# Performance work log

Measured on AMD Instinct MI355X. Metric: run time of the kernel, lower is better.

## Reference

```python
import jax, jax.numpy as jnp
import numpy as np

N_NODES = 20000
N_EDGES = 640000
IN_DIM, HIDDEN, OUT_DIM = 128, 256, 64
EPS = 1e-12


def setup_inputs() -> dict:
    key = jax.random.key(0)
    ks = jax.random.split(key, 8)
    x = jax.random.normal(ks[0], (N_NODES, IN_DIM), dtype=jnp.float32)
    edge_src = jax.random.randint(ks[1], (N_EDGES,), 0, N_NODES, dtype=jnp.int32)
    edge_dst = jax.random.randint(ks[2], (N_EDGES,), 0, N_NODES, dtype=jnp.int32)
    s1 = 1.0 / np.sqrt(IN_DIM)
    s2 = 1.0 / np.sqrt(HIDDEN)
    W1 = jax.random.uniform(ks[3], (IN_DIM, HIDDEN), jnp.float32, -s1, s1)
    b1 = jax.random.uniform(ks[4], (HIDDEN,), jnp.float32, -s1, s1)
    W2 = jax.random.uniform(ks[5], (HIDDEN, OUT_DIM), jnp.float32, -s2, s2)
    b2 = jax.random.uniform(ks[6], (OUT_DIM,), jnp.float32, -s2, s2)
    return {"x": x, "edge_src": edge_src, "edge_dst": edge_dst,
            "W1": W1, "b1": b1, "W2": W2, "b2": b2}


def _agnn_layer(h, src, dst, n_nodes):
    # AGNN propagation with beta = 1 (non-trainable buffer in source module):
    # out_i = sum_j softmax_j(cos(h_i, h_j)) * h_j over neighbors j (incl. self-loop)
    hn = h * jax.lax.rsqrt(jnp.sum(h * h, axis=-1, keepdims=True) + EPS)
    logits = jnp.sum(hn[src] * hn[dst], axis=-1)            # [E] cosine similarity
    m = jax.ops.segment_max(logits, dst, num_segments=n_nodes)
    e = jnp.exp(logits - m[dst])
    z = jax.ops.segment_sum(e, dst, num_segments=n_nodes)
    alpha = e / z[dst]                                       # per-dst softmax
    return jax.ops.segment_sum(alpha[:, None] * h[src], dst, num_segments=n_nodes)


def reference(x, edge_src, edge_dst, W1, b1, W2, b2):
    n = x.shape[0]
    loop = jnp.arange(n, dtype=edge_src.dtype)
    src = jnp.concatenate([edge_src, loop])
    dst = jnp.concatenate([edge_dst, loop])
    h = jax.nn.relu(x @ W1 + b1)
    for _ in range(4):
        h = jax.nn.relu(_agnn_layer(h, src, dst, n))
    return h @ W2 + b2
```

## Files before the change

### kernel.cpp

```cpp
#include <hip/hip_runtime.h>

#define N_NODES 20000
#define N_EDGES 640000
#define E_TOT   (N_EDGES + N_NODES)
#define IN_DIM  128
#define HIDDEN  256
#define OUT_DIM 64
#define LOG2E 1.4426950408889634f
#define NBIN 1024

typedef __attribute__((ext_vector_type(2))) float f32x2;

__device__ __forceinline__ unsigned short f2bf(float f) {
    union { float f; unsigned int i; } x; x.f = f;
    unsigned int u = x.i;
    return (unsigned short)((u + 0x7fffu + ((u >> 16) & 1u)) >> 16);
}
__device__ __forceinline__ f32x2 up2(unsigned int p) {
    f32x2 r;
    r.x = __uint_as_float(p << 16);
    r.y = __uint_as_float(p & 0xffff0000u);
    return r;
}
__device__ __forceinline__ unsigned int pk2(float a, float b) {
    return (unsigned int)f2bf(a) | ((unsigned int)f2bf(b) << 16);
}


__global__ void zero_all_kernel(int* __restrict__ cnt, int* __restrict__ hcur) {
    int i = blockIdx.x * blockDim.x + threadIdx.x;
    if (i < N_NODES) cnt[i] = 0;
    if (i < NBIN) hcur[i] = 0;
}

__global__ void count_kernel(const int* __restrict__ edge_dst, int* __restrict__ cnt) {
    int i = blockIdx.x * blockDim.x + threadIdx.x;
    if (i >= E_TOT) return;
    int d = (i < N_EDGES) ? edge_dst[i] : (i - N_EDGES);
    atomicAdd(&cnt[d], 1);
}

__global__ __launch_bounds__(1024) void scan_fused_kernel(int* __restrict__ cnt,
                                                          int* __restrict__ indptr,
                                                          int* __restrict__ hbase) {
    const int T = 1024;
    const int C = (N_NODES + T - 1) / T;
    __shared__ int sums[T];
    __shared__ int hist[T];
    int t = threadIdx.x;
    hist[t] = 0;
    __syncthreads();
    int base = t * C;
    int local[C];
    int s = 0;
#pragma unroll
    for (int i = 0; i < C; i++) {
        int idx = base + i;
        int v = 0;
        if (idx < N_NODES) {
            v = cnt[idx];
            int k = (v > NBIN - 1) ? (NBIN - 1) : v;
            atomicAdd(&hist[NBIN - 1 - k], 1);
        }
        local[i] = s;
        s += v;
    }
    sums[t] = s;
    __syncthreads();
    for (int off = 1; off < T; off <<= 1) {
        int v = (t >= off) ? sums[t - off] : 0;
        __syncthreads();
        sums[t] += v;
        __syncthreads();
    }
    int prefix = (t == 0) ? 0 : sums[t - 1];
#pragma unroll
    for (int i = 0; i < C; i++) {
        int idx = base + i;
        if (idx < N_NODES) {
            indptr[idx] = prefix + local[i];
            cnt[idx] = 0;
        }
    }
    if (t == T - 1) indptr[N_NODES] = prefix + s;
    __syncthreads();
    int hv = hist[t];
    sums[t] = hv;
    __syncthreads();
    for (int off = 1; off < T; off <<= 1) {
        int v = (t >= off) ? sums[t - off] : 0;
        __syncthreads();
        sums[t] += v;
        __syncthreads();
    }
    hbase[t] = sums[t] - hv;
}

__global__ void scatter_both_kernel(const int* __restrict__ edge_src,
                                    const int* __restrict__ edge_dst,
                                    const int* __restrict__ indptr,
                                    int* __restrict__ cnt,
                                    int* __restrict__ ssrc,
                                    const int* __restrict__ hbase,
                                    int* __restrict__ hcur,
                                    int* __restrict__ perm) {
    int i = blockIdx.x * blockDim.x + threadIdx.x;
    if (i < E_TOT) {
        int d, s;
        if (i < N_EDGES) { d = edge_dst[i]; s = edge_src[i]; }
        else             { d = i - N_EDGES; s = d; }
        int pos = indptr[d] + atomicAdd(&cnt[d], 1);
        ssrc[pos] = s;
    } else if (i < E_TOT + N_NODES) {
        int nidx = i - E_TOT;
        int d = indptr[nidx + 1] - indptr[nidx];
        int k = (d > NBIN - 1) ? (NBIN - 1) : d;
        int key = NBIN - 1 - k;
        int pos = hbase[key] + atomicAdd(&hcur[key], 1);
        perm[pos] = nidx;
    }
}


__global__ __launch_bounds__(256) void gemm_bias_act(const float* __restrict__ A,
                                                     const float* __restrict__ B,
                                                     const float* __restrict__ bias,
                                                     float* __restrict__ C,
                                                     int M, int Nn, int K, int relu) {
    __shared__ float As[16][65];
    __shared__ float Bs[16][65];
    int tid = threadIdx.x;
    int tx = tid & 15, ty = tid >> 4;
    int row0 = blockIdx.x * 64, col0 = blockIdx.y * 64;
    float acc[4][4] = {};
    for (int k0 = 0; k0 < K; k0 += 16) {
        {
            int r_ = tid >> 2;
            int kq = (tid & 3) * 4;
            int gr = row0 + r_;
            float4 a4 = make_float4(0.f, 0.f, 0.f, 0.f);
            if (gr < M) a4 = *(const float4*)&A[(long)gr * K + k0 + kq];
            As[kq + 0][r_] = a4.x; As[kq + 1][r_] = a4.y;
            As[kq + 2][r_] = a4.z; As[kq + 3][r_] = a4.w;
        }
        {
            int kr = tid >> 4;
            int cq = (tid & 15) * 4;
            float4 b4 = *(const float4*)&B[(long)(k0 + kr) * Nn + col0 + cq];
            Bs[kr][cq + 0] = b4.x; Bs[kr][cq + 1] = b4.y;
            Bs[kr][cq + 2] = b4.z; Bs[kr][cq + 3] = b4.w;
        }
        __syncthreads();
#pragma unroll
        for (int kk = 0; kk < 16; kk++) {
            float a[4], b[4];
#pragma unroll
            for (int i = 0; i < 4; i++) a[i] = As[kk][ty * 4 + i];
#pragma unroll
            for (int j = 0; j < 4; j++) b[j] = Bs[kk][tx * 4 + j];
#pragma unroll
            for (int i = 0; i < 4; i++)
#pragma unroll
                for (int j = 0; j < 4; j++) acc[i][j] += a[i] * b[j];
        }
        __syncthreads();
    }
#pragma unroll
    for (int i = 0; i < 4; i++) {
        int gr = row0 + ty * 4 + i;
        if (gr >= M) continue;
#pragma unroll
        for (int j = 0; j < 4; j++) {
            int gc = col0 + tx * 4 + j;
            float v = acc[i][j] + bias[gc];
            if (relu) v = fmaxf(v, 0.f);
            C[(long)gr * Nn + gc] = v;
        }
    }
}


__global__ __launch_bounds__(256) void normalize0_kernel(const float* __restrict__ h,
                                                         unsigned short* __restrict__ hnb,
                                                         float* __restrict__ r) {
    int wid = threadIdx.x >> 6, lane = threadIdx.x & 63;
    int i = blockIdx.x * 4 + wid;
    const float4* h4 = (const float4*)(h + (long)i * HIDDEN);
    float4 v = h4[lane];
    float ss = v.x * v.x + v.y * v.y + v.z * v.z + v.w * v.w;
#pragma unroll
    for (int off = 32; off; off >>= 1) ss += __shfl_xor(ss, off);
    float rr = sqrtf(ss + 1e-12f);
    float ir = 1.f / rr;
    uint2 o;
    o.x = pk2(v.x * ir, v.y * ir);
    o.y = pk2(v.z * ir, v.w * ir);
    ((uint2*)(hnb + (long)i * HIDDEN))[lane] = o;
    if (lane == 0) r[i] = rr;
}


__global__ __launch_bounds__(256) void agnn_kernel(const unsigned short* __restrict__ hnb,
                                                   const float* __restrict__ rin,
                                                   const int* __restrict__ indptr,
                                                   const int* __restrict__ ssrc,
                                                   const int* __restrict__ perm,
                                                   unsigned short* __restrict__ hnout,
                                                   float* __restrict__ rout,
                                                   float* __restrict__ hout,
                                                   int write_hn) {
    int lane = threadIdx.x & 63;
    int wid  = threadIdx.x >> 6;
    int half = lane >> 5;
    int sub  = (lane >> 4) & 1;
    int gl   = lane & 15;
    int node = perm[blockIdx.x * 8 + wid * 2 + half];

    const uint4* tab4 = (const uint4*)hnb;
    long nb = (long)node * 32 + gl * 2;
    uint4 ha = tab4[nb], hb = tab4[nb + 1];
    f32x2 hd2[8];
    hd2[0] = up2(ha.x) * LOG2E; hd2[1] = up2(ha.y) * LOG2E;
    hd2[2] = up2(ha.z) * LOG2E; hd2[3] = up2(ha.w) * LOG2E;
    hd2[4] = up2(hb.x) * LOG2E; hd2[5] = up2(hb.y) * LOG2E;
    hd2[6] = up2(hb.z) * LOG2E; hd2[7] = up2(hb.w) * LOG2E;

    int beg = indptr[node], end = indptr[node + 1];
    int deg = end - beg;
    int c0  = (deg + 1) >> 1;
    int cnt = sub ? (deg - c0) : c0;
    int eb  = beg + (sub ? c0 : 0);
    int lim = (cnt > 0) ? (eb + cnt - 1) : beg;
    int nmax = max(cnt, __shfl_xor(cnt, 16));
    nmax = max(nmax, __shfl_xor(nmax, 32));

    f32x2 acc[8];
#pragma unroll
    for (int p = 0; p < 8; p++) acc[p] = (f32x2)0.f;
    float z = 0.f;

    int s0 = ssrc[(0 < cnt) ? eb : lim];
    int s1 = ssrc[min(eb + 1, lim)];
    long b0 = (long)s0 * 32 + gl * 2;
    uint4 v0a = tab4[b0], v0b = tab4[b0 + 1];
    float r0 = rin[s0];
    long b1 = (long)s1 * 32 + gl * 2;
    uint4 v1a = tab4[b1], v1b = tab4[b1 + 1];
    float r1 = rin[s1];
    int s2 = ssrc[min(eb + 2, lim)];

    for (int i = 0; i < nmax; i++) {
        uint4 ca = v0a, cb = v0b;
        float cr = r0;
        v0a = v1a; v0b = v1b; r0 = r1;
        long b2 = (long)s2 * 32 + gl * 2;
        v1a = tab4[b2]; v1b = tab4[b2 + 1];
        r1 = rin[s2];
        s2 = ssrc[min(eb + i + 3, lim)];

        f32x2 cf[8];
        cf[0] = up2(ca.x); cf[1] = up2(ca.y); cf[2] = up2(ca.z); cf[3] = up2(ca.w);
        cf[4] = up2(cb.x); cf[5] = up2(cb.y); cf[6] = up2(cb.z); cf[7] = up2(cb.w);
        f32x2 da = cf[0] * hd2[0];
        f32x2 db = cf[1] * hd2[1];
        da += cf[2] * hd2[2];  db += cf[3] * hd2[3];
        da += cf[4] * hd2[4];  db += cf[5] * hd2[5];
        da += cf[6] * hd2[6];  db += cf[7] * hd2[7];
        f32x2 d2 = da + db;
        float d = d2.x + d2.y;
        d += __shfl_xor(d, 1);
        d += __shfl_xor(d, 2);
        d += __shfl_xor(d, 4);
        d += __shfl_xor(d, 8);
        float w = (i < cnt) ? exp2f(d) : 0.f;
        z += w;
        float wr = w * cr;
#pragma unroll
        for (int p = 0; p < 8; p++) acc[p] += cf[p] * wr;
    }

    z += __shfl_xor(z, 16);
#pragma unroll
    for (int p = 0; p < 8; p++) {
        acc[p].x += __shfl_xor(acc[p].x, 16);
        acc[p].y += __shfl_xor(acc[p].y, 16);
    }

    float inv = 1.f / z;
    f32x2 o[8];
#pragma unroll
    for (int p = 0; p < 8; p++) {
        f32x2 t = acc[p] * inv;
        t.x = fmaxf(t.x, 0.f);
        t.y = fmaxf(t.y, 0.f);
        o[p] = t;
    }

    if (write_hn) {
        float ss = 0.f;
#pragma unroll
        for (int p = 0; p < 8; p++) ss += o[p].x * o[p].x + o[p].y * o[p].y;
        ss += __shfl_xor(ss, 1);
        ss += __shfl_xor(ss, 2);
        ss += __shfl_xor(ss, 4);
        ss += __shfl_xor(ss, 8);
        float rr = sqrtf(ss + 1e-12f);
        float ir = 1.f / rr;
        if (sub == 0) {
            uint4 oa, ob;
            oa.x = pk2(o[0].x * ir, o[0].y * ir);
            oa.y = pk2(o[1].x * ir, o[1].y * ir);
            oa.z = pk2(o[2].x * ir, o[2].y * ir);
            oa.w = pk2(o[3].x * ir, o[3].y * ir);
            ob.x = pk2(o[4].x * ir, o[4].y * ir);
            ob.y = pk2(o[5].x * ir, o[5].y * ir);
            ob.z = pk2(o[6].x * ir, o[6].y * ir);
            ob.w = pk2(o[7].x * ir, o[7].y * ir);
            uint4* outt = (uint4*)hnout;
            outt[nb] = oa;
            outt[nb + 1] = ob;
            if (gl == 0) rout[node] = rr;
        }
    } else {
        if (sub == 0) {
            float4* ho = (float4*)(hout + (long)node * HIDDEN + gl * 16);
            ho[0] = make_float4(o[0].x, o[0].y, o[1].x, o[1].y);
            ho[1] = make_float4(o[2].x, o[2].y, o[3].x, o[3].y);
            ho[2] = make_float4(o[4].x, o[4].y, o[5].x, o[5].y);
            ho[3] = make_float4(o[6].x, o[6].y, o[7].x, o[7].y);
        }
    }
}


extern "C" void kernel_launch(void* const* d_in, const int* in_sizes, int n_in,
                              void* d_out, int out_size, void* d_ws, size_t ws_size,
                              hipStream_t stream) {
    const float* x  = (const float*)d_in[0];
    const int* esrc = (const int*)d_in[1];
    const int* edst = (const int*)d_in[2];
    const float* W1 = (const float*)d_in[3];
    const float* b1 = (const float*)d_in[4];
    const float* W2 = (const float*)d_in[5];
    const float* b2 = (const float*)d_in[6];
    float* out = (float*)d_out;

    char* ws = (char*)d_ws;
    float*          h0     = (float*)(ws);
    unsigned short* hnA    = (unsigned short*)(ws + 20480000);
    unsigned short* hnB    = (unsigned short*)(ws + 30720000);
    float*          rA     = (float*)(ws + 40960000);
    float*          rB     = (float*)(ws + 41040000);
    int*            indptr = (int*)  (ws + 41120000);
    int*            cnt    = (int*)  (ws + 41200256);
    int*            ssrc   = (int*)  (ws + 41280256);
    int*            perm   = (int*)  (ws + 43920256);
    int*            hbase  = (int*)  (ws + 44000256);
    int*            hcur   = (int*)  (ws + 44004352);

    zero_all_kernel<<<(N_NODES + 255) / 256, 256, 0, stream>>>(cnt, hcur);
    count_kernel<<<(E_TOT + 255) / 256, 256, 0, stream>>>(edst, cnt);
    scan_fused_kernel<<<1, 1024, 0, stream>>>(cnt, indptr, hbase);
    scatter_both_kernel<<<(E_TOT + N_NODES + 255) / 256, 256, 0, stream>>>(
        esrc, edst, indptr, cnt, ssrc, hbase, hcur, perm);

    dim3 g1((N_NODES + 63) / 64, HIDDEN / 64);
    gemm_bias_act<<<g1, 256, 0, stream>>>(x, W1, b1, h0, N_NODES, HIDDEN, IN_DIM, 1);

    normalize0_kernel<<<N_NODES / 4, 256, 0, stream>>>(h0, hnA, rA);

    int nblk = N_NODES / 8;
    agnn_kernel<<<nblk, 256, 0, stream>>>(hnA, rA, indptr, ssrc, perm, hnB, rB, h0, 1);
    agnn_kernel<<<nblk, 256, 0, stream>>>(hnB, rB, indptr, ssrc, perm, hnA, rA, h0, 1);
    agnn_kernel<<<nblk, 256, 0, stream>>>(hnA, rA, indptr, ssrc, perm, hnB, rB, h0, 1);
    agnn_kernel<<<nblk, 256, 0, stream>>>(hnB, rB, indptr, ssrc, perm, hnA, rA, h0, 0);

    dim3 g2((N_NODES + 63) / 64, OUT_DIM / 64);
    gemm_bias_act<<<g2, 256, 0, stream>>>(h0, W2, b2, out, N_NODES, OUT_DIM, HIDDEN, 0);
}
```

Baseline: 358.4 us.

## Shard CSR-build counters and assign one wave per node in AGNN

```diff
diff --git a/kernel.cpp b/kernel.cpp
--- a/kernel.cpp
+++ b/kernel.cpp
@@ -8,6 +8,7 @@
 #define OUT_DIM 64
 #define LOG2E 1.4426950408889634f
 #define NBIN 1024
+#define NSHARD 8
 
 typedef __attribute__((ext_vector_type(2))) float f32x2;
 
@@ -27,26 +28,27 @@
 }
 
 
-__global__ void zero_all_kernel(int* __restrict__ cnt, int* __restrict__ hcur) {
+__global__ void zero_all_kernel(int* __restrict__ cnt8, int* __restrict__ hcur) {
     int i = blockIdx.x * blockDim.x + threadIdx.x;
-    if (i < N_NODES) cnt[i] = 0;
+    if (i < NSHARD * N_NODES) cnt8[i] = 0;
     if (i < NBIN) hcur[i] = 0;
 }
 
-__global__ void count_kernel(const int* __restrict__ edge_dst, int* __restrict__ cnt) {
+__global__ void count_kernel(const int* __restrict__ edge_dst, int* __restrict__ cnt8) {
     int i = blockIdx.x * blockDim.x + threadIdx.x;
     if (i >= E_TOT) return;
+    int shard = blockIdx.x & (NSHARD - 1);
     int d = (i < N_EDGES) ? edge_dst[i] : (i - N_EDGES);
-    atomicAdd(&cnt[d], 1);
-}
-
-__global__ __launch_bounds__(1024) void scan_fused_kernel(int* __restrict__ cnt,
+    atomicAdd(&cnt8[shard * N_NODES + d], 1);
+}
+
+__global__ __launch_bounds__(1024) void scan_fused_kernel(int* __restrict__ cnt8,
                                                           int* __restrict__ indptr,
                                                           int* __restrict__ hbase) {
     const int T = 1024;
     const int C = (N_NODES + T - 1) / T;
     __shared__ int sums[T];
-    __shared__ int hist[T];
+    __shared__ int hist[NBIN];
     int t = threadIdx.x;
     hist[t] = 0;
     __syncthreads();
@@ -56,14 +58,15 @@
 #pragma unroll
     for (int i = 0; i < C; i++) {
         int idx = base + i;
-        int v = 0;
+        int deg = 0;
         if (idx < N_NODES) {
-            v = cnt[idx];
-            int k = (v > NBIN - 1) ? (NBIN - 1) : v;
+#pragma unroll
+            for (int s8 = 0; s8 < NSHARD; s8++) deg += cnt8[s8 * N_NODES + idx];
+            int k = (deg > NBIN - 1) ? (NBIN - 1) : deg;
             atomicAdd(&hist[NBIN - 1 - k], 1);
         }
         local[i] = s;
-        s += v;
+        s += deg;
     }
     sums[t] = s;
     __syncthreads();
@@ -78,8 +81,15 @@
     for (int i = 0; i < C; i++) {
         int idx = base + i;
         if (idx < N_NODES) {
-            indptr[idx] = prefix + local[i];
-            cnt[idx] = 0;
+            int ip = prefix + local[i];
+            indptr[idx] = ip;
+            int running = ip;
+#pragma unroll
+            for (int s8 = 0; s8 < NSHARD; s8++) {
+                int c = cnt8[s8 * N_NODES + idx];
+                cnt8[s8 * N_NODES + idx] = running;
+                running += c;
+            }
         }
     }
     if (t == T - 1) indptr[N_NODES] = prefix + s;
@@ -99,17 +109,18 @@
 __global__ void scatter_both_kernel(const int* __restrict__ edge_src,
                                     const int* __restrict__ edge_dst,
                                     const int* __restrict__ indptr,
-                                    int* __restrict__ cnt,
+                                    int* __restrict__ cnt8,
                                     int* __restrict__ ssrc,
                                     const int* __restrict__ hbase,
                                     int* __restrict__ hcur,
                                     int* __restrict__ perm) {
     int i = blockIdx.x * blockDim.x + threadIdx.x;
     if (i < E_TOT) {
+        int shard = blockIdx.x & (NSHARD - 1);
         int d, s;
         if (i < N_EDGES) { d = edge_dst[i]; s = edge_src[i]; }
         else             { d = i - N_EDGES; s = d; }
-        int pos = indptr[d] + atomicAdd(&cnt[d], 1);
+        int pos = atomicAdd(&cnt8[shard * N_NODES + d], 1);
         ssrc[pos] = s;
     } else if (i < E_TOT + N_NODES) {
         int nidx = i - E_TOT;
@@ -211,10 +222,9 @@
                                                    int write_hn) {
     int lane = threadIdx.x & 63;
     int wid  = threadIdx.x >> 6;
-    int half = lane >> 5;
-    int sub  = (lane >> 4) & 1;
+    int sub  = lane >> 4;
     int gl   = lane & 15;
-    int node = perm[blockIdx.x * 8 + wid * 2 + half];
+    int node = perm[blockIdx.x * 4 + wid];
 
     const uint4* tab4 = (const uint4*)hnb;
     long nb = (long)node * 32 + gl * 2;
@@ -227,9 +237,9 @@
 
     int beg = indptr[node], end = indptr[node + 1];
     int deg = end - beg;
-    int c0  = (deg + 1) >> 1;
-    int cnt = sub ? (deg - c0) : c0;
-    int eb  = beg + (sub ? c0 : 0);
+    int qb  = deg >> 2, rem = deg & 3;
+    int cnt = qb + (sub < rem ? 1 : 0);
+    int eb  = beg + sub * qb + min(sub, rem);
     int lim = (cnt > 0) ? (eb + cnt - 1) : beg;
     int nmax = max(cnt, __shfl_xor(cnt, 16));
     nmax = max(nmax, __shfl_xor(nmax, 32));
@@ -280,10 +290,13 @@
     }
 
     z += __shfl_xor(z, 16);
+    z += __shfl_xor(z, 32);
 #pragma unroll
     for (int p = 0; p < 8; p++) {
         acc[p].x += __shfl_xor(acc[p].x, 16);
         acc[p].y += __shfl_xor(acc[p].y, 16);
+        acc[p].x += __shfl_xor(acc[p].x, 32);
+        acc[p].y += __shfl_xor(acc[p].y, 32);
     }
 
     float inv = 1.f / z;
@@ -352,24 +365,24 @@
     float*          rA     = (float*)(ws + 40960000);
     float*          rB     = (float*)(ws + 41040000);
     int*            indptr = (int*)  (ws + 41120000);
-    int*            cnt    = (int*)  (ws + 41200256);
-    int*            ssrc   = (int*)  (ws + 41280256);
-    int*            perm   = (int*)  (ws + 43920256);
-    int*            hbase  = (int*)  (ws + 44000256);
-    int*            hcur   = (int*)  (ws + 44004352);
-
-    zero_all_kernel<<<(N_NODES + 255) / 256, 256, 0, stream>>>(cnt, hcur);
-    count_kernel<<<(E_TOT + 255) / 256, 256, 0, stream>>>(edst, cnt);
-    scan_fused_kernel<<<1, 1024, 0, stream>>>(cnt, indptr, hbase);
+    int*            cnt8   = (int*)  (ws + 41200256);
+    int*            ssrc   = (int*)  (ws + 41840256);
+    int*            perm   = (int*)  (ws + 44480256);
+    int*            hbase  = (int*)  (ws + 44560256);
+    int*            hcur   = (int*)  (ws + 44564352);
+
+    zero_all_kernel<<<(NSHARD * N_NODES + 255) / 256, 256, 0, stream>>>(cnt8, hcur);
+    count_kernel<<<(E_TOT + 255) / 256, 256, 0, stream>>>(edst, cnt8);
+    scan_fused_kernel<<<1, 1024, 0, stream>>>(cnt8, indptr, hbase);
     scatter_both_kernel<<<(E_TOT + N_NODES + 255) / 256, 256, 0, stream>>>(
-        esrc, edst, indptr, cnt, ssrc, hbase, hcur, perm);
+        esrc, edst, indptr, cnt8, ssrc, hbase, hcur, perm);
 
     dim3 g1((N_NODES + 63) / 64, HIDDEN / 64);
     gemm_bias_act<<<g1, 256, 0, stream>>>(x, W1, b1, h0, N_NODES, HIDDEN, IN_DIM, 1);
 
     normalize0_kernel<<<N_NODES / 4, 256, 0, stream>>>(h0, hnA, rA);
 
-    int nblk = N_NODES / 8;
+    int nblk = N_NODES / 4;
     agnn_kernel<<<nblk, 256, 0, stream>>>(hnA, rA, indptr, ssrc, perm, hnB, rB, h0, 1);
     agnn_kernel<<<nblk, 256, 0, stream>>>(hnB, rB, indptr, ssrc, perm, hnA, rA, h0, 1);
     agnn_kernel<<<nblk, 256, 0, stream>>>(hnA, rA, indptr, ssrc, perm, hnB, rB, h0, 1);
```

Result: slower. 511.6 us (+42.7%).
